# Kernel tuning notes

Measured on AMD Instinct MI355X. Metric: run time of the kernel, lower is better.

Reference implementation:

```python
import jax, jax.numpy as jnp
import numpy as np

B, L, D = 4, 512, 1024
E, TOP_K = 16, 4
F = 4 * D  # expert hidden width


def setup_inputs() -> dict:
    key = jax.random.key(0)
    ks = jax.random.split(key, 6)
    scale = 0.02
    return {
        "x": jax.random.normal(ks[0], (B, L, D), jnp.float32),
        "keys": jax.random.normal(ks[1], (E, D), jnp.float32),          # expert_keys
        "w1": jax.random.normal(ks[2], (E, F, D), jnp.float32) * scale,  # Linear(D,4D).weight per expert
        "b1": jnp.zeros((E, F), jnp.float32),
        "w2": jax.random.normal(ks[3], (E, D, F), jnp.float32) * scale,  # Linear(4D,D).weight per expert
        "b2": jnp.zeros((E, D), jnp.float32),
        "rw": jax.random.normal(ks[4], (E, D), jnp.float32) * scale,     # router Linear(D,E).weight
        "rb": jnp.zeros((E,), jnp.float32),
    }


def reference(x, keys, w1, b1, w2, b2, rw, rb):
    # Laplace gate: squared Euclidean distance token-to-expert-key (broadcasted, as in torch)
    diff = x[:, :, None, :] - keys                      # (B,L,E,D)
    dist2 = jnp.sum(diff * diff, axis=-1)               # (B,L,E)
    logits = -dist2 + jnp.einsum('bld,ed->ble', x, rw) + rb

    topv, topi = jax.lax.top_k(logits, TOP_K)           # (B,L,K)
    w = jax.nn.softmax(topv, axis=-1)                   # (B,L,K)

    # Dense all-expert MLP (exact GELU, matching torch nn.GELU default)
    hidden = jax.nn.gelu(jnp.einsum('bld,efd->blef', x, w1) + b1, approximate=False)  # (B,L,E,F)
    exp_out = jnp.einsum('blef,edf->bled', hidden, w2) + b2                            # (B,L,E,D)

    # Gather top-k expert outputs and combine with softmax weights
    sel = jnp.take_along_axis(exp_out, topi[..., None], axis=2)  # (B,L,K,D)
    fused = jnp.sum(w[..., None] * sel, axis=2)                  # (B,L,D)
    return fused
```

## Files before the change

### kernel.cpp

```cpp
#include <hip/hip_runtime.h>

#define B_ 4
#define L_ 512
#define D_ 1024
#define E_ 16
#define K_ 4
#define F_ 4096
#define NTOK (B_*L_)
#define NPAIR (NTOK*K_)

typedef float f32x4 __attribute__((ext_vector_type(4)));
typedef __bf16 bf16x8 __attribute__((ext_vector_type(8)));

__device__ inline unsigned int pack2(float a, float b) {
    unsigned short ua = __builtin_bit_cast(unsigned short, (__bf16)a);
    unsigned short ub = __builtin_bit_cast(unsigned short, (__bf16)b);
    return (unsigned int)ua | ((unsigned int)ub << 16);
}

#define GLOAD16(g, l) __builtin_amdgcn_global_load_lds( \
    (const __attribute__((address_space(1))) void*)(g), \
    (__attribute__((address_space(3))) void*)(l), 16, 0, 0)

__global__ __launch_bounds__(256) void cvt_kernel(const float* __restrict__ src,
                                                  unsigned short* __restrict__ dst)
{
    size_t i = ((size_t)blockIdx.x * 256 + threadIdx.x) * 16;
    const float4* s = reinterpret_cast<const float4*>(src + i);
    float4 v0 = s[0], v1 = s[1], v2 = s[2], v3 = s[3];
    uint4 p0 = { pack2(v0.x,v0.y), pack2(v0.z,v0.w), pack2(v1.x,v1.y), pack2(v1.z,v1.w) };
    uint4 p1 = { pack2(v2.x,v2.y), pack2(v2.z,v2.w), pack2(v3.x,v3.y), pack2(v3.z,v3.w) };
    uint4* d = reinterpret_cast<uint4*>(dst + i);
    d[0] = p0; d[1] = p1;
}

__global__ __launch_bounds__(256) void router_kernel(
    const float* __restrict__ x, const float* __restrict__ keys,
    const float* __restrict__ rw, const float* __restrict__ rb,
    int* __restrict__ topi, float* __restrict__ topw, int* __restrict__ counts)
{
    int t = blockIdx.x;
    int tid = threadIdx.x;
    if (blockIdx.x == 0 && tid < E_) counts[tid] = 0;

    __shared__ float xs[D_];
    const float* xrow = x + (size_t)t * D_;
    for (int i = tid; i < D_; i += 256) xs[i] = xrow[i];
    __syncthreads();

    int e    = tid >> 4;
    int lane = tid & 15;
    const float* krow = keys + e * D_;
    const float* rrow = rw   + e * D_;
    double dist2 = 0.0, dot = 0.0;
    for (int d = lane; d < D_; d += 16) {
        float xv = xs[d];
        float df = xv - krow[d];
        dist2 += (double)df * df;
        dot   += (double)xv * rrow[d];
    }
    #pragma unroll
    for (int m = 8; m >= 1; m >>= 1) {
        dist2 += __shfl_xor(dist2, m);
        dot   += __shfl_xor(dot, m);
    }
    __shared__ float lg[E_];
    if (lane == 0) lg[e] = (float)(-dist2 + dot) + rb[e];
    __syncthreads();

    if (tid == 0) {
        float v[E_];
        #pragma unroll
        for (int i = 0; i < E_; i++) v[i] = lg[i];
        int   idx[K_]; float val[K_];
        #pragma unroll
        for (int k = 0; k < K_; k++) {
            int bi = 0; float bv = -1e30f;
            #pragma unroll
            for (int i = 0; i < E_; i++) if (v[i] > bv) { bv = v[i]; bi = i; }
            idx[k] = bi; val[k] = bv; v[bi] = -1e30f;
        }
        float mx = val[0], s = 0.f, w[K_];
        #pragma unroll
        for (int k = 0; k < K_; k++) { w[k] = expf(val[k] - mx); s += w[k]; }
        float inv = 1.0f / s;
        #pragma unroll
        for (int k = 0; k < K_; k++) {
            topi[t*K_ + k] = idx[k];
            topw[t*K_ + k] = w[k] * inv;
        }
    }
}

__global__ void bucket_kernel(const int* __restrict__ topi, const float* __restrict__ topw,
                              int* __restrict__ counts,
                              int* __restrict__ bucket_tok, float* __restrict__ bucket_w)
{
    int i = blockIdx.x * 256 + threadIdx.x;
    if (i >= NPAIR) return;
    int t = i >> 2;
    int e = topi[i];
    int pos = atomicAdd(&counts[e], 1);
    bucket_tok[e * NTOK + pos] = t;
    bucket_w [e * NTOK + pos] = topw[i];
}

__global__ void scan_kernel(const int* __restrict__ counts, int* __restrict__ offsets)
{
    if (threadIdx.x == 0) {
        int s = 0;
        for (int e = 0; e < E_; e++) { offsets[e] = s; s += counts[e]; }
        offsets[E_] = s;
    }
}

__global__ __launch_bounds__(256) void gemm1_kernel(
    const unsigned short* __restrict__ xb, const unsigned short* __restrict__ w1b,
    const float* __restrict__ b1,
    const int* __restrict__ counts, const int* __restrict__ offsets,
    const int* __restrict__ bucket_tok, unsigned short* __restrict__ hidden)
{
    int e  = blockIdx.z;
    int Te = counts[e];
    int row0 = blockIdx.y * 128;
    if (row0 >= Te) return;
    int f0 = blockIdx.x * 128;
    int tid = threadIdx.x;
    int lane = tid & 63, wave = tid >> 6;

    __shared__ unsigned short As[128][32];
    __shared__ unsigned short Bs[128][32];
    __shared__ int toks[128];

    if (tid < 128) {
        int r = row0 + tid;
        toks[tid] = bucket_tok[e * NTOK + (r < Te ? r : Te - 1)];
    }
    __syncthreads();

    int sl = lane & 3;
    int r0 = (wave * 2 + 0) * 16 + (lane >> 2);
    int r1 = (wave * 2 + 1) * 16 + (lane >> 2);
    const unsigned short* pa0 = xb + (size_t)toks[r0] * D_ + sl * 8;
    const unsigned short* pa1 = xb + (size_t)toks[r1] * D_ + sl * 8;
    const unsigned short* pb0 = w1b + ((size_t)e * F_ + f0 + r0) * D_ + sl * 8;
    const unsigned short* pb1 = w1b + ((size_t)e * F_ + f0 + r1) * D_ + sl * 8;
    unsigned short* la0 = &As[(wave * 2 + 0) * 16][0];
    unsigned short* la1 = &As[(wave * 2 + 1) * 16][0];
    unsigned short* lb0 = &Bs[(wave * 2 + 0) * 16][0];
    unsigned short* lb1 = &Bs[(wave * 2 + 1) * 16][0];

    int wr = wave >> 1, wc = wave & 1;
    int lr = lane & 15, ko = (lane >> 4) * 8;

    f32x4 acc[4][4];
    #pragma unroll
    for (int m = 0; m < 4; m++)
        #pragma unroll
        for (int n = 0; n < 4; n++) acc[m][n] = (f32x4){0.f, 0.f, 0.f, 0.f};

    for (int k0 = 0; k0 < D_; k0 += 32) {
        GLOAD16(pa0 + k0, la0);
        GLOAD16(pa1 + k0, la1);
        GLOAD16(pb0 + k0, lb0);
        GLOAD16(pb1 + k0, lb1);
        __syncthreads();
        bf16x8 a[4], b[4];
        #pragma unroll
        for (int m = 0; m < 4; m++) a[m] = *reinterpret_cast<const bf16x8*>(&As[wr*64 + m*16 + lr][ko]);
        #pragma unroll
        for (int n = 0; n < 4; n++) b[n] = *reinterpret_cast<const bf16x8*>(&Bs[wc*64 + n*16 + lr][ko]);
        #pragma unroll
        for (int m = 0; m < 4; m++)
            #pragma unroll
            for (int n = 0; n < 4; n++)
                acc[m][n] = __builtin_amdgcn_mfma_f32_16x16x32_bf16(a[m], b[n], acc[m][n], 0, 0, 0);
        __syncthreads();
    }

    int obase = offsets[e];
    #pragma unroll
    for (int m = 0; m < 4; m++) {
        int rbase = wr*64 + m*16 + (lane >> 4) * 4;
        #pragma unroll
        for (int n = 0; n < 4; n++) {
            int gcol = f0 + wc*64 + n*16 + lr;
            float bias = b1[e * F_ + gcol];
            #pragma unroll
            for (int r = 0; r < 4; r++) {
                int lrow = rbase + r;
                if (row0 + lrow < Te) {
                    float v = acc[m][n][r] + bias;
                    float g = 0.5f * v * (1.0f + erff(v * 0.70710678118654752f));
                    hidden[(size_t)(obase + row0 + lrow) * F_ + gcol] =
                        __builtin_bit_cast(unsigned short, (__bf16)g);
                }
            }
        }
    }
}

__global__ __launch_bounds__(256) void gemm2_kernel(
    const unsigned short* __restrict__ hidden, const unsigned short* __restrict__ w2b,
    const float* __restrict__ b2,
    const int* __restrict__ counts, const int* __restrict__ offsets,
    const int* __restrict__ bucket_tok, const float* __restrict__ bucket_w,
    float* __restrict__ out)
{
    int e  = blockIdx.z;
    int Te = counts[e];
    int row0 = blockIdx.y * 128;
    if (row0 >= Te) return;
    int n0 = blockIdx.x * 128;
    int tid = threadIdx.x;
    int lane = tid & 63, wave = tid >> 6;

    __shared__ unsigned short As[128][32];
    __shared__ unsigned short Bs[128][32];
    __shared__ int   toks[128];
    __shared__ float wts [128];

    int obase = offsets[e];
    if (tid < 128) {
        int r = row0 + tid;
        int rc = (r < Te ? r : Te - 1);
        toks[tid] = bucket_tok[e * NTOK + rc];
        wts [tid] = bucket_w [e * NTOK + rc];
    }
    __syncthreads();

    int sl = lane & 3;
    int r0 = (wave * 2 + 0) * 16 + (lane >> 2);
    int r1 = (wave * 2 + 1) * 16 + (lane >> 2);
    int ar0 = row0 + r0; ar0 = (ar0 < Te ? ar0 : Te - 1);
    int ar1 = row0 + r1; ar1 = (ar1 < Te ? ar1 : Te - 1);
    const unsigned short* pa0 = hidden + (size_t)(obase + ar0) * F_ + sl * 8;
    const unsigned short* pa1 = hidden + (size_t)(obase + ar1) * F_ + sl * 8;
    const unsigned short* pb0 = w2b + ((size_t)e * D_ + n0 + r0) * F_ + sl * 8;
    const unsigned short* pb1 = w2b + ((size_t)e * D_ + n0 + r1) * F_ + sl * 8;
    unsigned short* la0 = &As[(wave * 2 + 0) * 16][0];
    unsigned short* la1 = &As[(wave * 2 + 1) * 16][0];
    unsigned short* lb0 = &Bs[(wave * 2 + 0) * 16][0];
    unsigned short* lb1 = &Bs[(wave * 2 + 1) * 16][0];

    int wr = wave >> 1, wc = wave & 1;
    int lr = lane & 15, ko = (lane >> 4) * 8;

    f32x4 acc[4][4];
    #pragma unroll
    for (int m = 0; m < 4; m++)
        #pragma unroll
        for (int n = 0; n < 4; n++) acc[m][n] = (f32x4){0.f, 0.f, 0.f, 0.f};

    for (int k0 = 0; k0 < F_; k0 += 32) {
        GLOAD16(pa0 + k0, la0);
        GLOAD16(pa1 + k0, la1);
        GLOAD16(pb0 + k0, lb0);
        GLOAD16(pb1 + k0, lb1);
        __syncthreads();
        bf16x8 a[4], b[4];
        #pragma unroll
        for (int m = 0; m < 4; m++) a[m] = *reinterpret_cast<const bf16x8*>(&As[wr*64 + m*16 + lr][ko]);
        #pragma unroll
        for (int n = 0; n < 4; n++) b[n] = *reinterpret_cast<const bf16x8*>(&Bs[wc*64 + n*16 + lr][ko]);
        #pragma unroll
        for (int m = 0; m < 4; m++)
            #pragma unroll
            for (int n = 0; n < 4; n++)
                acc[m][n] = __builtin_amdgcn_mfma_f32_16x16x32_bf16(a[m], b[n], acc[m][n], 0, 0, 0);
        __syncthreads();
    }

    #pragma unroll
    for (int m = 0; m < 4; m++) {
        int rbase = wr*64 + m*16 + (lane >> 4) * 4;
        #pragma unroll
        for (int n = 0; n < 4; n++) {
            int gcol = n0 + wc*64 + n*16 + lr;
            float bias = b2[e * D_ + gcol];
            #pragma unroll
            for (int r = 0; r < 4; r++) {
                int lrow = rbase + r;
                if (row0 + lrow < Te) {
                    float v = acc[m][n][r] + bias;
                    atomicAdd(&out[(size_t)toks[lrow] * D_ + gcol], wts[lrow] * v);
                }
            }
        }
    }
}

extern "C" void kernel_launch(void* const* d_in, const int* in_sizes, int n_in,
                              void* d_out, int out_size, void* d_ws, size_t ws_size,
                              hipStream_t stream)
{
    const float* x    = (const float*)d_in[0];
    const float* keys = (const float*)d_in[1];
    const float* w1   = (const float*)d_in[2];
    const float* b1   = (const float*)d_in[3];
    const float* w2   = (const float*)d_in[4];
    const float* b2   = (const float*)d_in[5];
    const float* rw   = (const float*)d_in[6];
    const float* rb   = (const float*)d_in[7];
    float* out = (float*)d_out;

    char* wsp = (char*)d_ws;
    size_t off = 0;
    auto alloc = [&](size_t bytes) -> char* {
        char* p = wsp + off;
        off = (off + bytes + 255) & ~(size_t)255;
        return p;
    };
    int*   topi       = (int*)  alloc(NPAIR * sizeof(int));
    float* topw       = (float*)alloc(NPAIR * sizeof(float));
    int*   counts     = (int*)  alloc(E_ * sizeof(int));
    int*   offsets    = (int*)  alloc((E_ + 1) * sizeof(int));
    int*   bucket_tok = (int*)  alloc((size_t)E_ * NTOK * sizeof(int));
    float* bucket_w   = (float*)alloc((size_t)E_ * NTOK * sizeof(float));
    unsigned short* xb     = (unsigned short*)alloc((size_t)NTOK * D_ * sizeof(unsigned short));
    unsigned short* w1b    = (unsigned short*)alloc((size_t)E_ * F_ * D_ * sizeof(unsigned short));
    unsigned short* w2b    = (unsigned short*)alloc((size_t)E_ * D_ * F_ * sizeof(unsigned short));
    unsigned short* hidden = (unsigned short*)alloc((size_t)NPAIR * F_ * sizeof(unsigned short));

    hipMemsetAsync(d_out, 0, (size_t)out_size * sizeof(float), stream);

    router_kernel<<<NTOK, 256, 0, stream>>>(x, keys, rw, rb, topi, topw, counts);
    bucket_kernel<<<NPAIR / 256, 256, 0, stream>>>(topi, topw, counts, bucket_tok, bucket_w);
    scan_kernel<<<1, 64, 0, stream>>>(counts, offsets);

    cvt_kernel<<<(NTOK * D_) / 4096, 256, 0, stream>>>(x, xb);
    cvt_kernel<<<(E_ * F_ * D_) / 4096, 256, 0, stream>>>(w1, w1b);
    cvt_kernel<<<(E_ * D_ * F_) / 4096, 256, 0, stream>>>(w2, w2b);

    gemm1_kernel<<<dim3(F_ / 128, NTOK / 128, E_), 256, 0, stream>>>(
        xb, w1b, b1, counts, offsets, bucket_tok, hidden);
    gemm2_kernel<<<dim3(D_ / 128, NTOK / 128, E_), 256, 0, stream>>>(
        hidden, w2b, b2, counts, offsets, bucket_tok, bucket_w, out);
}
```

Before: 993.5 us.

## Double-buffer LDS with swizzled K=64 tiles and XCD-aware block remap in expert GEMMs

```diff
diff --git a/kernel.cpp b/kernel.cpp
--- a/kernel.cpp
+++ b/kernel.cpp
@@ -21,6 +21,11 @@
 #define GLOAD16(g, l) __builtin_amdgcn_global_load_lds( \
     (const __attribute__((address_space(1))) void*)(g), \
     (__attribute__((address_space(3))) void*)(l), 16, 0, 0)
+
+__device__ inline int xcdmap(int orig, int nwg) {
+    int q = nwg >> 3;
+    return (orig & 7) * q + (orig >> 3);
+}
 
 __global__ __launch_bounds__(256) void cvt_kernel(const float* __restrict__ src,
                                                   unsigned short* __restrict__ dst)
@@ -114,22 +119,24 @@
     }
 }
 
-__global__ __launch_bounds__(256) void gemm1_kernel(
+#define G1_BLOCKS (16*32*16)
+__global__ __launch_bounds__(256, 2) void gemm1_kernel(
     const unsigned short* __restrict__ xb, const unsigned short* __restrict__ w1b,
     const float* __restrict__ b1,
     const int* __restrict__ counts, const int* __restrict__ offsets,
     const int* __restrict__ bucket_tok, unsigned short* __restrict__ hidden)
 {
-    int e  = blockIdx.z;
+    int id = xcdmap(blockIdx.x, G1_BLOCKS);
+    int y = id & 15, n = (id >> 4) & 31, e = id >> 9;
     int Te = counts[e];
-    int row0 = blockIdx.y * 128;
+    int row0 = y * 128;
     if (row0 >= Te) return;
-    int f0 = blockIdx.x * 128;
+    int f0 = n * 128;
     int tid = threadIdx.x;
-    int lane = tid & 63, wave = tid >> 6;
-
-    __shared__ unsigned short As[128][32];
-    __shared__ unsigned short Bs[128][32];
+    int lane = tid & 63, w = tid >> 6;
+
+    __shared__ unsigned short As[2][128][64];
+    __shared__ unsigned short Bs[2][128][64];
     __shared__ int toks[128];
 
     if (tid < 128) {
@@ -138,59 +145,86 @@
     }
     __syncthreads();
 
-    int sl = lane & 3;
-    int r0 = (wave * 2 + 0) * 16 + (lane >> 2);
-    int r1 = (wave * 2 + 1) * 16 + (lane >> 2);
-    const unsigned short* pa0 = xb + (size_t)toks[r0] * D_ + sl * 8;
-    const unsigned short* pa1 = xb + (size_t)toks[r1] * D_ + sl * 8;
-    const unsigned short* pb0 = w1b + ((size_t)e * F_ + f0 + r0) * D_ + sl * 8;
-    const unsigned short* pb1 = w1b + ((size_t)e * F_ + f0 + r1) * D_ + sl * 8;
-    unsigned short* la0 = &As[(wave * 2 + 0) * 16][0];
-    unsigned short* la1 = &As[(wave * 2 + 1) * 16][0];
-    unsigned short* lb0 = &Bs[(wave * 2 + 0) * 16][0];
-    unsigned short* lb1 = &Bs[(wave * 2 + 1) * 16][0];
-
-    int wr = wave >> 1, wc = wave & 1;
-    int lr = lane & 15, ko = (lane >> 4) * 8;
+    int lr3 = (lane >> 3) & 7;
+    int slg = (lane & 7) ^ lr3;
+    const unsigned short* pa[4];
+    const unsigned short* pb[4];
+    unsigned short* da[4];
+    unsigned short* db[4];
+    #pragma unroll
+    for (int b = 0; b < 4; b++) {
+        int row = 32 * b + 8 * w + lr3;
+        pa[b] = xb  + (size_t)toks[row] * D_ + slg * 8;
+        pb[b] = w1b + ((size_t)e * F_ + f0 + row) * D_ + slg * 8;
+        da[b] = &As[0][32 * b + 8 * w][0];
+        db[b] = &Bs[0][32 * b + 8 * w][0];
+    }
+    const size_t bufstep = 128 * 64;
+
+    int lr = lane & 15, q = lane >> 4;
+    int col0 = ((q ^ (lr & 7)) * 8);
+    int wr = w >> 1, wc = w & 1;
 
     f32x4 acc[4][4];
     #pragma unroll
     for (int m = 0; m < 4; m++)
         #pragma unroll
-        for (int n = 0; n < 4; n++) acc[m][n] = (f32x4){0.f, 0.f, 0.f, 0.f};
-
-    for (int k0 = 0; k0 < D_; k0 += 32) {
-        GLOAD16(pa0 + k0, la0);
-        GLOAD16(pa1 + k0, la1);
-        GLOAD16(pb0 + k0, lb0);
-        GLOAD16(pb1 + k0, lb1);
+        for (int nn = 0; nn < 4; nn++) acc[m][nn] = (f32x4){0.f,0.f,0.f,0.f};
+
+    #define G1_STAGE(nb, k0) { \
+        _Pragma("unroll") \
+        for (int b = 0; b < 4; b++) { \
+            GLOAD16(pa[b] + (k0), da[b] + (nb) * bufstep); \
+            GLOAD16(pb[b] + (k0), db[b] + (nb) * bufstep); \
+        } }
+
+    #define G1_COMPUTE(cb) { \
+        bf16x8 af[4][2], bfr[4][2]; \
+        _Pragma("unroll") \
+        for (int m = 0; m < 4; m++) { \
+            int r = wr*64 + m*16 + lr; \
+            af[m][0] = *reinterpret_cast<const bf16x8*>(&As[cb][r][col0]); \
+            af[m][1] = *reinterpret_cast<const bf16x8*>(&As[cb][r][col0 ^ 32]); \
+        } \
+        _Pragma("unroll") \
+        for (int nn = 0; nn < 4; nn++) { \
+            int r = wc*64 + nn*16 + lr; \
+            bfr[nn][0] = *reinterpret_cast<const bf16x8*>(&Bs[cb][r][col0]); \
+            bfr[nn][1] = *reinterpret_cast<const bf16x8*>(&Bs[cb][r][col0 ^ 32]); \
+        } \
+        _Pragma("unroll") \
+        for (int kk = 0; kk < 2; kk++) \
+            _Pragma("unroll") \
+            for (int m = 0; m < 4; m++) \
+                _Pragma("unroll") \
+                for (int nn = 0; nn < 4; nn++) \
+                    acc[m][nn] = __builtin_amdgcn_mfma_f32_16x16x32_bf16(af[m][kk], bfr[nn][kk], acc[m][nn], 0, 0, 0); \
+        }
+
+    G1_STAGE(0, 0);
+    __syncthreads();
+    int cur = 0;
+    for (int kt = 1; kt < D_ / 64; ++kt) {
+        G1_STAGE(cur ^ 1, kt * 64);
+        G1_COMPUTE(cur);
         __syncthreads();
-        bf16x8 a[4], b[4];
-        #pragma unroll
-        for (int m = 0; m < 4; m++) a[m] = *reinterpret_cast<const bf16x8*>(&As[wr*64 + m*16 + lr][ko]);
-        #pragma unroll
-        for (int n = 0; n < 4; n++) b[n] = *reinterpret_cast<const bf16x8*>(&Bs[wc*64 + n*16 + lr][ko]);
-        #pragma unroll
-        for (int m = 0; m < 4; m++)
-            #pragma unroll
-            for (int n = 0; n < 4; n++)
-                acc[m][n] = __builtin_amdgcn_mfma_f32_16x16x32_bf16(a[m], b[n], acc[m][n], 0, 0, 0);
-        __syncthreads();
-    }
+        cur ^= 1;
+    }
+    G1_COMPUTE(cur);
 
     int obase = offsets[e];
     #pragma unroll
     for (int m = 0; m < 4; m++) {
-        int rbase = wr*64 + m*16 + (lane >> 4) * 4;
-        #pragma unroll
-        for (int n = 0; n < 4; n++) {
-            int gcol = f0 + wc*64 + n*16 + lr;
+        int rbase = wr*64 + m*16 + q * 4;
+        #pragma unroll
+        for (int nn = 0; nn < 4; nn++) {
+            int gcol = f0 + wc*64 + nn*16 + lr;
             float bias = b1[e * F_ + gcol];
             #pragma unroll
             for (int r = 0; r < 4; r++) {
                 int lrow = rbase + r;
                 if (row0 + lrow < Te) {
-                    float v = acc[m][n][r] + bias;
+                    float v = acc[m][nn][r] + bias;
                     float g = 0.5f * v * (1.0f + erff(v * 0.70710678118654752f));
                     hidden[(size_t)(obase + row0 + lrow) * F_ + gcol] =
                         __builtin_bit_cast(unsigned short, (__bf16)g);
@@ -200,23 +234,25 @@
     }
 }
 
-__global__ __launch_bounds__(256) void gemm2_kernel(
+#define G2_BLOCKS (16*8*16)
+__global__ __launch_bounds__(256, 2) void gemm2_kernel(
     const unsigned short* __restrict__ hidden, const unsigned short* __restrict__ w2b,
     const float* __restrict__ b2,
     const int* __restrict__ counts, const int* __restrict__ offsets,
     const int* __restrict__ bucket_tok, const float* __restrict__ bucket_w,
     float* __restrict__ out)
 {
-    int e  = blockIdx.z;
+    int id = xcdmap(blockIdx.x, G2_BLOCKS);
+    int y = id & 15, n = (id >> 4) & 7, e = id >> 7;
     int Te = counts[e];
-    int row0 = blockIdx.y * 128;
+    int row0 = y * 128;
     if (row0 >= Te) return;
-    int n0 = blockIdx.x * 128;
+    int n0 = n * 128;
     int tid = threadIdx.x;
-    int lane = tid & 63, wave = tid >> 6;
-
-    __shared__ unsigned short As[128][32];
-    __shared__ unsigned short Bs[128][32];
+    int lane = tid & 63, w = tid >> 6;
+
+    __shared__ unsigned short As[2][128][64];
+    __shared__ unsigned short Bs[2][128][64];
     __shared__ int   toks[128];
     __shared__ float wts [128];
 
@@ -229,60 +265,56 @@
     }
     __syncthreads();
 
-    int sl = lane & 3;
-    int r0 = (wave * 2 + 0) * 16 + (lane >> 2);
-    int r1 = (wave * 2 + 1) * 16 + (lane >> 2);
-    int ar0 = row0 + r0; ar0 = (ar0 < Te ? ar0 : Te - 1);
-    int ar1 = row0 + r1; ar1 = (ar1 < Te ? ar1 : Te - 1);
-    const unsigned short* pa0 = hidden + (size_t)(obase + ar0) * F_ + sl * 8;
-    const unsigned short* pa1 = hidden + (size_t)(obase + ar1) * F_ + sl * 8;
-    const unsigned short* pb0 = w2b + ((size_t)e * D_ + n0 + r0) * F_ + sl * 8;
-    const unsigned short* pb1 = w2b + ((size_t)e * D_ + n0 + r1) * F_ + sl * 8;
-    unsigned short* la0 = &As[(wave * 2 + 0) * 16][0];
-    unsigned short* la1 = &As[(wave * 2 + 1) * 16][0];
-    unsigned short* lb0 = &Bs[(wave * 2 + 0) * 16][0];
-    unsigned short* lb1 = &Bs[(wave * 2 + 1) * 16][0];
-
-    int wr = wave >> 1, wc = wave & 1;
-    int lr = lane & 15, ko = (lane >> 4) * 8;
+    int lr3 = (lane >> 3) & 7;
+    int slg = (lane & 7) ^ lr3;
+    const unsigned short* pa[4];
+    const unsigned short* pb[4];
+    unsigned short* da[4];
+    unsigned short* db[4];
+    #pragma unroll
+    for (int b = 0; b < 4; b++) {
+        int row = 32 * b + 8 * w + lr3;
+        int ar = row0 + row; ar = (ar < Te ? ar : Te - 1);
+        pa[b] = hidden + (size_t)(obase + ar) * F_ + slg * 8;
+        pb[b] = w2b + ((size_t)e * D_ + n0 + row) * F_ + slg * 8;
+        da[b] = &As[0][32 * b + 8 * w][0];
+        db[b] = &Bs[0][32 * b + 8 * w][0];
+    }
+    const size_t bufstep = 128 * 64;
+
+    int lr = lane & 15, q = lane >> 4;
+    int col0 = ((q ^ (lr & 7)) * 8);
+    int wr = w >> 1, wc = w & 1;
 
     f32x4 acc[4][4];
     #pragma unroll
     for (int m = 0; m < 4; m++)
         #pragma unroll
-        for (int n = 0; n < 4; n++) acc[m][n] = (f32x4){0.f, 0.f, 0.f, 0.f};
-
-    for (int k0 = 0; k0 < F_; k0 += 32) {
-        GLOAD16(pa0 + k0, la0);
-        GLOAD16(pa1 + k0, la1);
-        GLOAD16(pb0 + k0, lb0);
-        GLOAD16(pb1 + k0, lb1);
+        for (int nn = 0; nn < 4; nn++) acc[m][nn] = (f32x4){0.f,0.f,0.f,0.f};
+
+    G1_STAGE(0, 0);
+    __syncthreads();
+    int cur = 0;
+    for (int kt = 1; kt < F_ / 64; ++kt) {
+        G1_STAGE(cur ^ 1, kt * 64);
+        G1_COMPUTE(cur);
         __syncthreads();
-        bf16x8 a[4], b[4];
-        #pragma unroll
-        for (int m = 0; m < 4; m++) a[m] = *reinterpret_cast<const bf16x8*>(&As[wr*64 + m*16 + lr][ko]);
-        #pragma unroll
-        for (int n = 0; n < 4; n++) b[n] = *reinterpret_cast<const bf16x8*>(&Bs[wc*64 + n*16 + lr][ko]);
-        #pragma unroll
-        for (int m = 0; m < 4; m++)
-            #pragma unroll
-            for (int n = 0; n < 4; n++)
-                acc[m][n] = __builtin_amdgcn_mfma_f32_16x16x32_bf16(a[m], b[n], acc[m][n], 0, 0, 0);
-        __syncthreads();
-    }
+        cur ^= 1;
+    }
+    G1_COMPUTE(cur);
 
     #pragma unroll
     for (int m = 0; m < 4; m++) {
-        int rbase = wr*64 + m*16 + (lane >> 4) * 4;
-        #pragma unroll
-        for (int n = 0; n < 4; n++) {
-            int gcol = n0 + wc*64 + n*16 + lr;
+        int rbase = wr*64 + m*16 + q * 4;
+        #pragma unroll
+        for (int nn = 0; nn < 4; nn++) {
+            int gcol = n0 + wc*64 + nn*16 + lr;
             float bias = b2[e * D_ + gcol];
             #pragma unroll
             for (int r = 0; r < 4; r++) {
                 int lrow = rbase + r;
                 if (row0 + lrow < Te) {
-                    float v = acc[m][n][r] + bias;
+                    float v = acc[m][nn][r] + bias;
                     atomicAdd(&out[(size_t)toks[lrow] * D_ + gcol], wts[lrow] * v);
                 }
             }
@@ -332,8 +364,8 @@
     cvt_kernel<<<(E_ * F_ * D_) / 4096, 256, 0, stream>>>(w1, w1b);
     cvt_kernel<<<(E_ * D_ * F_) / 4096, 256, 0, stream>>>(w2, w2b);
 
-    gemm1_kernel<<<dim3(F_ / 128, NTOK / 128, E_), 256, 0, stream>>>(
+    gemm1_kernel<<<G1_BLOCKS, 256, 0, stream>>>(
         xb, w1b, b1, counts, offsets, bucket_tok, hidden);
-    gemm2_kernel<<<dim3(D_ / 128, NTOK / 128, E_), 256, 0, stream>>>(
+    gemm2_kernel<<<G2_BLOCKS, 256, 0, stream>>>(
         hidden, w2b, b2, counts, offsets, bucket_tok, bucket_w, out);
 }
```

Measured after the change: 1.283 ms. +29.1%, slower.
